# Kernel tuning notes

Measured on AMD Instinct MI355X. Metric: run time of the kernel, lower is better.

## Reference

```python
import jax, jax.numpy as jnp
import numpy as np

B = 8192
IN = 2048   # input_size
H = 2048    # hidden_size
D = IN + H  # combine feature dim = 4096


def setup_inputs() -> dict:
    key = jax.random.key(0)
    ks = jax.random.split(key, 11)
    s = 1.0 / np.sqrt(D)  # nn.Linear default init scale
    inp = {
        "input": jax.random.normal(ks[0], (B, D), jnp.float32),
        "hidden": jax.random.normal(ks[1], (B, D), jnp.float32),
        "cell": jax.random.normal(ks[2], (B, H), jnp.float32),
        "Wf": jax.random.uniform(ks[3], (D, H), jnp.float32, -s, s),
        "bf": jax.random.uniform(ks[4], (H,), jnp.float32, -s, s),
        "Wc": jax.random.uniform(ks[5], (D, H), jnp.float32, -s, s),
        "bc": jax.random.uniform(ks[6], (H,), jnp.float32, -s, s),
        "Wi": jax.random.uniform(ks[7], (D, H), jnp.float32, -s, s),
        "bi": jax.random.uniform(ks[8], (H,), jnp.float32, -s, s),
        "Wo": jax.random.uniform(ks[9], (D, H), jnp.float32, -s, s),
        "bo": jax.random.uniform(ks[10], (H,), jnp.float32, -s, s),
    }
    return inp


def reference(input, hidden, cell, Wf, bf, Wc, bc, Wi, bi, Wo, bo):
    combine = input + hidden  # [B, D] elementwise add (as in source, not concat)
    # Fuse the 4 gate GEMMs into one [D, 4H] GEMM for efficiency (same math).
    W = jnp.concatenate([Wf, Wc, Wi, Wo], axis=1)  # [D, 4H]
    b = jnp.concatenate([bf, bc, bi, bo])          # [4H]
    gates = combine @ W + b                        # [B, 4H]
    gf, gc, gi, go = jnp.split(gates, 4, axis=1)
    ft = jax.nn.sigmoid(gf)
    ct_ = jnp.tanh(gc)
    it = jax.nn.sigmoid(jax.nn.sigmoid(gi))  # double sigmoid, faithful to source
    cell_state = cell * ft + ct_ * it
    out = jax.nn.sigmoid(go)
    hidden_state = out * jnp.tanh(cell_state)
    return (out, hidden_state, cell_state)
```

## Files before the change

### kernel.cpp

```cpp
#include <hip/hip_runtime.h>
#include <hip/hip_bf16.h>

#define B_SZ 8192
#define D_SZ 4096
#define H_SZ 2048
#define N4H  8192
#define NT   (D_SZ / 64)

typedef __attribute__((ext_vector_type(8))) __bf16 bf16x8;
typedef __attribute__((ext_vector_type(4))) float f32x4;

#define GPTR(p) ((__attribute__((address_space(1))) void*)(p))
#define LPTR(p) ((__attribute__((address_space(3))) void*)(p))

__global__ void prep_k(const float* __restrict__ x, const float* __restrict__ h,
                       __hip_bfloat16* __restrict__ comb,
                       const float* __restrict__ Wf, const float* __restrict__ Wc,
                       const float* __restrict__ Wi, const float* __restrict__ Wo,
                       __hip_bfloat16* __restrict__ WT) {
    __shared__ float t[32][33];
    if (blockIdx.x < 2048) {
        const size_t n4 = (size_t)B_SZ * D_SZ / 4;
        const size_t stride = (size_t)2048 * 256;
        for (size_t i = (size_t)blockIdx.x * 256 + threadIdx.x; i < n4; i += stride) {
            f32x4 a = __builtin_nontemporal_load((const f32x4*)x + i);
            f32x4 b = __builtin_nontemporal_load((const f32x4*)h + i);
            short4 r;
            r.x = __builtin_bit_cast(short, __float2bfloat16(a.x + b.x));
            r.y = __builtin_bit_cast(short, __float2bfloat16(a.y + b.y));
            r.z = __builtin_bit_cast(short, __float2bfloat16(a.z + b.z));
            r.w = __builtin_bit_cast(short, __float2bfloat16(a.w + b.w));
            ((short4*)comb)[i] = r;
        }
    } else {
        const int b = blockIdx.x - 2048;
        const int k0 = (b & 127) * 32;
        const int n0 = (b >> 7) * 32;
        const float* W = (n0 < H_SZ) ? Wf : (n0 < 2 * H_SZ) ? Wc
                       : (n0 < 3 * H_SZ) ? Wi : Wo;
        const int g = n0 >> 11;
        const int nc = n0 & (H_SZ - 1);
        const int tx = threadIdx.x & 31, ty = threadIdx.x >> 5;
#pragma unroll
        for (int j = 0; j < 4; ++j)
            t[ty + j * 8][tx] = __builtin_nontemporal_load(
                W + (size_t)(k0 + ty + j * 8) * H_SZ + nc + tx);
        __syncthreads();
#pragma unroll
        for (int j = 0; j < 4; ++j) {
            const int h2 = nc + ty + j * 8;
            const int np = ((h2 >> 4) << 6) + (g << 4) + (h2 & 15);
            WT[(size_t)np * D_SZ + k0 + tx] = __float2bfloat16(t[tx][ty + j * 8]);
        }
    }
}


#define LDS_A0 0
#define LDS_A1 16384
#define LDS_BB0 32768
#define LDS_BB1 49152

#define BAR()                                    \
    do {                                         \
        asm volatile("" ::: "memory");           \
        __builtin_amdgcn_s_barrier();            \
        asm volatile("" ::: "memory");           \
    } while (0)

#define STAGE_A(h, kt)                                                                 \
    do {                                                                               \
        _Pragma("unroll") for (int c_ = 0; c_ < 4; ++c_) {                             \
            __builtin_amdgcn_global_load_lds(                                          \
                GPTR(pA + (size_t)((c_ >> 1) * 128 + (h) * 64 + (c_ & 1) * 32) * D_SZ  \
                         + (size_t)(kt) * 64),                                         \
                LPTR(smem + (h) * 16384 + c_ * 4096 + wave * 1024), 16, 0, 0);         \
        }                                                                              \
    } while (0)

#define STAGE_B(qn, kt, bb)                                                            \
    do {                                                                               \
        _Pragma("unroll") for (int c_ = 0; c_ < 2; ++c_) {                             \
            __builtin_amdgcn_global_load_lds(                                          \
                GPTR(pB + (size_t)((qn) * 32 + c_ * 64) * D_SZ + (size_t)(kt) * 64),   \
                LPTR(smem + (bb) + (qn) * 8192 + c_ * 4096 + wave * 1024), 16, 0, 0);  \
        }                                                                              \
    } while (0)

#define LDA(dst, RB)                                                                   \
    do {                                                                               \
        _Pragma("unroll") for (int mi = 0; mi < 4; ++mi) {                             \
            const int row_ = wr * 64 + mi * 16 + fr;                                   \
            dst[mi][0] = *(const bf16x8*)(smem + (RB) + row_ * 128 + sw0);             \
            dst[mi][1] = *(const bf16x8*)(smem + (RB) + row_ * 128 + sw1);             \
        }                                                                              \
    } while (0)

#define LDB(dst, BB, qn)                                                               \
    do {                                                                               \
        _Pragma("unroll") for (int nf = 0; nf < 2; ++nf) {                             \
            const int row_ = (qn) * 64 + wc * 32 + nf * 16 + fr;                       \
            dst[nf][0] = *(const bf16x8*)(smem + (BB) + row_ * 128 + sw0);             \
            dst[nf][1] = *(const bf16x8*)(smem + (BB) + row_ * 128 + sw1);             \
        }                                                                              \
    } while (0)

#define MFMA_Q(qm, qn, areg, breg)                                                     \
    do {                                                                               \
        _Pragma("unroll") for (int mi = 0; mi < 4; ++mi)                               \
        _Pragma("unroll") for (int nf = 0; nf < 2; ++nf)                               \
        _Pragma("unroll") for (int ks = 0; ks < 2; ++ks)                               \
            acc[(qm) * 4 + mi][(qn) * 2 + nf] =                                        \
                __builtin_amdgcn_mfma_f32_16x16x32_bf16(                               \
                    areg[mi][ks], breg[nf][ks],                                        \
                    acc[(qm) * 4 + mi][(qn) * 2 + nf], 0, 0, 0);                       \
    } while (0)

#define TILE(KT, CURB, OTHB)                                                           \
    {                                                                                  \
        const int kt_ = (KT) & 63;                                                     \
                        \
        LDA(a, LDS_A0);                                                                \
        LDB(b0, CURB, 0);                                                              \
        STAGE_B(0, kt_, OTHB);                                                         \
        __builtin_amdgcn_s_setprio(1);                                                 \
        MFMA_Q(0, 0, a, b0);                                                           \
        __builtin_amdgcn_s_setprio(0);                                                 \
        asm volatile("s_waitcnt vmcnt(6)" ::: "memory");                               \
        BAR();                                                                         \
                     \
        LDB(b1, CURB, 1);                                                              \
        STAGE_A(0, kt_);                                                               \
        __builtin_amdgcn_s_setprio(1);                                                 \
        MFMA_Q(0, 1, a, b1);                                                           \
        __builtin_amdgcn_s_setprio(0);                                                 \
        asm volatile("s_waitcnt vmcnt(6)" ::: "memory");                               \
        BAR();                                                                         \
                              \
        LDA(a, LDS_A1);                                                                \
        STAGE_B(1, kt_, OTHB);                                                         \
        __builtin_amdgcn_s_setprio(1);                                                 \
        MFMA_Q(1, 0, a, b0);                                                           \
        __builtin_amdgcn_s_setprio(0);                                                 \
        asm volatile("s_waitcnt vmcnt(6)" ::: "memory");                               \
        BAR();                                                                         \
                                  \
        STAGE_A(1, kt_);                                                               \
        __builtin_amdgcn_s_setprio(1);                                                 \
        MFMA_Q(1, 1, a, b1);                                                           \
        __builtin_amdgcn_s_setprio(0);                                                 \
        asm volatile("s_waitcnt vmcnt(6)" ::: "memory");                               \
        BAR();                                                                         \
    }

__device__ __forceinline__ float fsig(float x) { return 1.f / (1.f + __expf(-x)); }
__device__ __forceinline__ float ftanh(float x) {
    x = fminf(fmaxf(x, -15.f), 15.f);
    float e = __expf(2.f * x);
    return (e - 1.f) / (e + 1.f);
}

__global__ __launch_bounds__(256, 2) void gemm4_k(
    const __hip_bfloat16* __restrict__ A,
    const __hip_bfloat16* __restrict__ BT,
    const float* __restrict__ cell,
    const float* __restrict__ bfb, const float* __restrict__ bcb,
    const float* __restrict__ bib, const float* __restrict__ bob,
    float* __restrict__ out)
{
    extern __shared__ char smem[];

    const int tid  = threadIdx.x;
    const int wave = tid >> 6;
    const int lane = tid & 63;
    const int wr = wave >> 1;
    const int wc = wave & 1;
    const int fr = lane & 15;
    const int sw0 = (((lane >> 4) + 0) ^ (fr & 7)) << 4;
    const int sw1 = (((lane >> 4) + 4) ^ (fr & 7)) << 4;

    const int wg = (blockIdx.x & 7) * 256 + (blockIdx.x >> 3);
    const int ntile = wg & 63;
    const int m0 = (wg >> 6) * 256;
    const int n0 = ntile * 128;

    const int r0   = tid >> 3;
    const int col0 = ((tid & 7) ^ (r0 & 7)) << 3;
    const __hip_bfloat16* pA = A  + (size_t)(m0 + r0) * D_SZ + col0;
    const __hip_bfloat16* pB = BT + (size_t)(n0 + r0) * D_SZ + col0;

    f32x4 acc[8][4] = {};
    bf16x8 a[4][2], b0[2][2], b1[2][2];

    STAGE_B(0, 0, LDS_BB0);
    STAGE_A(0, 0);
    STAGE_B(1, 0, LDS_BB0);
    STAGE_A(1, 0);
    asm volatile("s_waitcnt vmcnt(6)" ::: "memory");
    BAR();

#pragma unroll 1
    for (int t = 0; t < NT; t += 2) {
        TILE(t + 1, LDS_BB0, LDS_BB1);
        TILE(t + 2, LDS_BB1, LDS_BB0);
    }

    {
        const int crow = (lane >> 4) * 4;
        const int ccol = lane & 15;
        const int hh = (ntile * 2 + wc) * 16 + ccol;
        const float bf_ = bfb[hh], bc_ = bcb[hh], bi_ = bib[hh], bo_ = bob[hh];
        const size_t BH = (size_t)B_SZ * H_SZ;
        float* hidp = out + BH;
        float* cstp = out + 2 * BH;
#pragma unroll
        for (int ai = 0; ai < 8; ++ai) {
#pragma unroll
            for (int j = 0; j < 4; ++j) {
                const size_t r = (size_t)(m0 + wr * 128 + ai * 16 + crow + j);
                const size_t idx = r * H_SZ + hh;
                const float gf = acc[ai][0][j] + bf_;
                const float gc = acc[ai][1][j] + bc_;
                const float gi = acc[ai][2][j] + bi_;
                const float go = acc[ai][3][j] + bo_;
                const float ft = fsig(gf);
                const float ct = ftanh(gc);
                const float it_ = fsig(fsig(gi));
                const float ot = fsig(go);
                const float cv = __builtin_nontemporal_load(cell + idx);
                const float cs = cv * ft + ct * it_;
                __builtin_nontemporal_store(ot, out + idx);
                __builtin_nontemporal_store(cs, cstp + idx);
                __builtin_nontemporal_store(ot * ftanh(cs), hidp + idx);
            }
        }
    }

    asm volatile("s_waitcnt vmcnt(0)" ::: "memory");
}

extern "C" void kernel_launch(void* const* d_in, const int* in_sizes, int n_in,
                              void* d_out, int out_size, void* d_ws, size_t ws_size,
                              hipStream_t stream) {
    const float* input  = (const float*)d_in[0];
    const float* hidden = (const float*)d_in[1];
    const float* cell   = (const float*)d_in[2];
    const float* Wf     = (const float*)d_in[3];
    const float* bfb    = (const float*)d_in[4];
    const float* Wc     = (const float*)d_in[5];
    const float* bcb    = (const float*)d_in[6];
    const float* Wi     = (const float*)d_in[7];
    const float* bib    = (const float*)d_in[8];
    const float* Wo     = (const float*)d_in[9];
    const float* bob    = (const float*)d_in[10];
    float* out = (float*)d_out;

    char* ws = (char*)d_ws;
    __hip_bfloat16* comb = (__hip_bfloat16*)ws;
    __hip_bfloat16* WT   = (__hip_bfloat16*)(ws + (size_t)B_SZ * D_SZ * 2);

    hipFuncSetAttribute(reinterpret_cast<const void*>(gemm4_k),
                        hipFuncAttributeMaxDynamicSharedMemorySize, 65536);

    prep_k<<<2048 + 32768, 256, 0, stream>>>(input, hidden, comb, Wf, Wc, Wi, Wo, WT);
    gemm4_k<<<2048, 256, 65536, stream>>>(comb, WT, cell, bfb, bcb, bib, bob, out);
}
```

Before: 597.7 us.

## Load B fragments directly from global into registers, double-buffer A in LDS

The B operand no longer goes through LDS. Each wave now loads its B fragments straight from global memory into double-buffered registers, one tile ahead. A is staged into two LDS buffers, and each k-tile runs with a single barrier instead of four quarter-step barriers. The aim is to cut LDS traffic and barrier stalls. The cost is more register pressure, duplicated global and L2 reads of B across waves that share columns, and exposed global-load latency. The final prefetch also reads one tile past the k range without masking.

```diff
diff --git a/kernel.cpp b/kernel.cpp
--- a/kernel.cpp
+++ b/kernel.cpp
@@ -56,11 +56,6 @@
 }
 
 
-#define LDS_A0 0
-#define LDS_A1 16384
-#define LDS_BB0 32768
-#define LDS_BB1 49152
-
 #define BAR()                                    \
     do {                                         \
         asm volatile("" ::: "memory");           \
@@ -68,22 +63,14 @@
         asm volatile("" ::: "memory");           \
     } while (0)
 
-#define STAGE_A(h, kt)                                                                 \
-    do {                                                                               \
+#define STAGE_A8(kt, BUF)                                                              \
+    do {                                                                               \
+        _Pragma("unroll") for (int h_ = 0; h_ < 2; ++h_)                               \
         _Pragma("unroll") for (int c_ = 0; c_ < 4; ++c_) {                             \
             __builtin_amdgcn_global_load_lds(                                          \
-                GPTR(pA + (size_t)((c_ >> 1) * 128 + (h) * 64 + (c_ & 1) * 32) * D_SZ  \
+                GPTR(pA + (size_t)((c_ >> 1) * 128 + h_ * 64 + (c_ & 1) * 32) * D_SZ   \
                          + (size_t)(kt) * 64),                                         \
-                LPTR(smem + (h) * 16384 + c_ * 4096 + wave * 1024), 16, 0, 0);         \
-        }                                                                              \
-    } while (0)
-
-#define STAGE_B(qn, kt, bb)                                                            \
-    do {                                                                               \
-        _Pragma("unroll") for (int c_ = 0; c_ < 2; ++c_) {                             \
-            __builtin_amdgcn_global_load_lds(                                          \
-                GPTR(pB + (size_t)((qn) * 32 + c_ * 64) * D_SZ + (size_t)(kt) * 64),   \
-                LPTR(smem + (bb) + (qn) * 8192 + c_ * 4096 + wave * 1024), 16, 0, 0);  \
+                LPTR(smem + (BUF) + h_ * 16384 + c_ * 4096 + wave * 1024), 16, 0, 0);  \
         }                                                                              \
     } while (0)
 
@@ -96,13 +83,12 @@
         }                                                                              \
     } while (0)
 
-#define LDB(dst, BB, qn)                                                               \
-    do {                                                                               \
-        _Pragma("unroll") for (int nf = 0; nf < 2; ++nf) {                             \
-            const int row_ = (qn) * 64 + wc * 32 + nf * 16 + fr;                       \
-            dst[nf][0] = *(const bf16x8*)(smem + (BB) + row_ * 128 + sw0);             \
-            dst[nf][1] = *(const bf16x8*)(smem + (BB) + row_ * 128 + sw1);             \
-        }                                                                              \
+#define LDB_G(dst, qn, kt)                                                             \
+    do {                                                                               \
+        _Pragma("unroll") for (int nf = 0; nf < 2; ++nf)                               \
+        _Pragma("unroll") for (int ks = 0; ks < 2; ++ks)                               \
+            dst[nf][ks] = *(const bf16x8*)(pBg                                         \
+                + (size_t)((qn) * 32 + nf * 16) * D_SZ + (size_t)(kt) * 64 + ks * 32); \
     } while (0)
 
 #define MFMA_Q(qm, qn, areg, breg)                                                     \
@@ -116,40 +102,23 @@
                     acc[(qm) * 4 + mi][(qn) * 2 + nf], 0, 0, 0);                       \
     } while (0)
 
-#define TILE(KT, CURB, OTHB)                                                           \
+#define TILE2(KTN, CUR, OTH, bc0, bc1, bn0, bn1)                                       \
     {                                                                                  \
-        const int kt_ = (KT) & 63;                                                     \
-                        \
-        LDA(a, LDS_A0);                                                                \
-        LDB(b0, CURB, 0);                                                              \
-        STAGE_B(0, kt_, OTHB);                                                         \
+        LDA(a, (CUR));                                                                 \
+        STAGE_A8((KTN), (OTH));                                                        \
+        asm volatile("" ::: "memory");             \
+        LDB_G(bn0, 0, (KTN));                                                          \
+        LDB_G(bn1, 1, (KTN));                                                          \
         __builtin_amdgcn_s_setprio(1);                                                 \
-        MFMA_Q(0, 0, a, b0);                                                           \
+        MFMA_Q(0, 0, a, bc0);                                                          \
+        MFMA_Q(0, 1, a, bc1);                                                          \
         __builtin_amdgcn_s_setprio(0);                                                 \
-        asm volatile("s_waitcnt vmcnt(6)" ::: "memory");                               \
-        BAR();                                                                         \
-                     \
-        LDB(b1, CURB, 1);                                                              \
-        STAGE_A(0, kt_);                                                               \
+        LDA(a, (CUR) + 16384);                                                         \
         __builtin_amdgcn_s_setprio(1);                                                 \
-        MFMA_Q(0, 1, a, b1);                                                           \
+        MFMA_Q(1, 0, a, bc0);                                                          \
+        MFMA_Q(1, 1, a, bc1);                                                          \
         __builtin_amdgcn_s_setprio(0);                                                 \
-        asm volatile("s_waitcnt vmcnt(6)" ::: "memory");                               \
-        BAR();                                                                         \
-                              \
-        LDA(a, LDS_A1);                                                                \
-        STAGE_B(1, kt_, OTHB);                                                         \
-        __builtin_amdgcn_s_setprio(1);                                                 \
-        MFMA_Q(1, 0, a, b0);                                                           \
-        __builtin_amdgcn_s_setprio(0);                                                 \
-        asm volatile("s_waitcnt vmcnt(6)" ::: "memory");                               \
-        BAR();                                                                         \
-                                  \
-        STAGE_A(1, kt_);                                                               \
-        __builtin_amdgcn_s_setprio(1);                                                 \
-        MFMA_Q(1, 1, a, b1);                                                           \
-        __builtin_amdgcn_s_setprio(0);                                                 \
-        asm volatile("s_waitcnt vmcnt(6)" ::: "memory");                               \
+        asm volatile("s_waitcnt vmcnt(8)" ::: "memory");          \
         BAR();                                                                         \
     }
 
@@ -176,8 +145,9 @@
     const int wr = wave >> 1;
     const int wc = wave & 1;
     const int fr = lane & 15;
-    const int sw0 = (((lane >> 4) + 0) ^ (fr & 7)) << 4;
-    const int sw1 = (((lane >> 4) + 4) ^ (fr & 7)) << 4;
+    const int hi = lane >> 4;
+    const int sw0 = ((hi + 0) ^ (fr & 7)) << 4;
+    const int sw1 = ((hi + 4) ^ (fr & 7)) << 4;
 
     const int wg = (blockIdx.x & 7) * 256 + (blockIdx.x >> 3);
     const int ntile = wg & 63;
@@ -186,28 +156,27 @@
 
     const int r0   = tid >> 3;
     const int col0 = ((tid & 7) ^ (r0 & 7)) << 3;
-    const __hip_bfloat16* pA = A  + (size_t)(m0 + r0) * D_SZ + col0;
-    const __hip_bfloat16* pB = BT + (size_t)(n0 + r0) * D_SZ + col0;
+    const __hip_bfloat16* pA = A + (size_t)(m0 + r0) * D_SZ + col0;
+    const __hip_bfloat16* pBg = BT + (size_t)(n0 + wc * 64 + fr) * D_SZ + hi * 8;
 
     f32x4 acc[8][4] = {};
-    bf16x8 a[4][2], b0[2][2], b1[2][2];
-
-    STAGE_B(0, 0, LDS_BB0);
-    STAGE_A(0, 0);
-    STAGE_B(1, 0, LDS_BB0);
-    STAGE_A(1, 0);
-    asm volatile("s_waitcnt vmcnt(6)" ::: "memory");
+    bf16x8 a[4][2], bA0[2][2], bA1[2][2], bB0[2][2], bB1[2][2];
+
+    STAGE_A8(0, 0);
+    asm volatile("s_waitcnt vmcnt(0)" ::: "memory");
     BAR();
+    LDB_G(bA0, 0, 0);
+    LDB_G(bA1, 1, 0);
 
 #pragma unroll 1
     for (int t = 0; t < NT; t += 2) {
-        TILE(t + 1, LDS_BB0, LDS_BB1);
-        TILE(t + 2, LDS_BB1, LDS_BB0);
+        TILE2(t + 1, 0,     32768, bA0, bA1, bB0, bB1);
+        TILE2(t + 2, 32768, 0,     bB0, bB1, bA0, bA1);
     }
 
     {
-        const int crow = (lane >> 4) * 4;
-        const int ccol = lane & 15;
+        const int crow = hi * 4;
+        const int ccol = fr;
         const int hh = (ntile * 2 + wc) * 16 + ccol;
         const float bf_ = bfb[hh], bc_ = bcb[hh], bi_ = bib[hh], bo_ = bob[hh];
         const size_t BH = (size_t)B_SZ * H_SZ;
```

New measurement: 799.1 us. +33.7%, slower.
